# Kernel optimization log

Hardware: AMD Instinct MI355X
Metric: run time of the kernel (lower is better)

The kernel has to match this reference:

```python
import jax, jax.numpy as jnp
import numpy as np

NUM_HEADS = 4
INITIAL_VALUE = 1.0
HEADS_RANGE = 3.0


def rotate_every_two(x):
    x1 = x[..., ::2]
    x2 = x[..., 1::2]
    return jnp.stack([-x2, x1], axis=-1).reshape(x.shape)


def theta_shift(x, sin, cos):
    return x * cos + rotate_every_two(x) * sin


def rel_pos_2d(h, w, key_dim):
    # angle: repeat each frequency twice -> length key_dim
    base = 1.0 / 10000.0 ** jnp.linspace(0.0, 1.0, key_dim // 2)
    angle = jnp.repeat(base, 2)
    decay = jnp.log(1.0 - 2.0 ** (-(INITIAL_VALUE + HEADS_RANGE * jnp.arange(NUM_HEADS, dtype=jnp.float32) / NUM_HEADS)))
    idx = jnp.arange(h * w, dtype=jnp.float32)
    sin = jnp.sin(idx[:, None] * angle[None, :]).reshape(h, w, key_dim)
    cos = jnp.cos(idx[:, None] * angle[None, :]).reshape(h, w, key_dim)
    def decay_1d(l):
        i = jnp.arange(l, dtype=jnp.float32)
        return jnp.abs(i[:, None] - i[None, :])[None, :, :] * decay[:, None, None]  # (n, l, l)
    return sin, cos, decay_1d(h), decay_1d(w)


def setup_inputs() -> dict:
    key = jax.random.key(0)
    b, C, H, W = 16, 256, 64, 64
    ks = jax.random.split(key, 12)
    gain = 2.0 ** (-2.5)
    xav = (2.0 / (C + C)) ** 0.5
    return {
        "x": jax.random.normal(ks[0], (b, C, H, W), jnp.float32),
        "Wq": jax.random.normal(ks[1], (C, C), jnp.float32) * gain * xav,
        "bq": jnp.zeros((C,), jnp.float32),
        "Wk": jax.random.normal(ks[2], (C, C), jnp.float32) * gain * xav,
        "bk": jnp.zeros((C,), jnp.float32),
        "Wv": jax.random.normal(ks[3], (C, C), jnp.float32) * gain * xav,
        "bv": jnp.zeros((C,), jnp.float32),
        "dw_kernel": jax.random.normal(ks[4], (5, 5, 1, C), jnp.float32) * 0.05,
        "dw_bias": jnp.zeros((C,), jnp.float32),
        "Wo": jax.random.normal(ks[5], (C, C), jnp.float32) * xav,
        "bo": jnp.zeros((C,), jnp.float32),
    }


def reference(x, Wq, bq, Wk, bk, Wv, bv, dw_kernel, dw_bias, Wo, bo):
    x = jnp.transpose(x, (0, 2, 3, 1))  # (b, h, w, c)
    b, h, w, c = x.shape
    n = NUM_HEADS
    d = c // n  # key_dim == head_dim (value_factor=1)
    scaling = d ** (-0.5)

    sin, cos, mask_h, mask_w = rel_pos_2d(h, w, d)

    q = x @ Wq + bq
    k = (x @ Wk + bk) * scaling
    v = x @ Wv + bv  # (b, h, w, c)

    # depthwise 5x5 conv (lepe) on v, NHWC
    lepe = jax.lax.conv_general_dilated(
        v, dw_kernel, window_strides=(1, 1), padding=((2, 2), (2, 2)),
        dimension_numbers=("NHWC", "HWIO", "NHWC"), feature_group_count=c,
    ) + dw_bias

    q = q.reshape(b, h, w, n, d).transpose(0, 3, 1, 2, 4)  # (b, n, h, w, d)
    k = k.reshape(b, h, w, n, d).transpose(0, 3, 1, 2, 4)
    qr = theta_shift(q, sin, cos)  # sin/cos (h,w,d) broadcast
    kr = theta_shift(k, sin, cos)

    # width-axis attention: rows independent
    qr_w = qr.transpose(0, 2, 1, 3, 4)  # (b, h, n, w, d)
    kr_w = kr.transpose(0, 2, 1, 3, 4)
    v5 = v.reshape(b, h, w, n, d).transpose(0, 1, 3, 2, 4)  # (b, h, n, w, d)
    qk_w = jnp.einsum("bhnqd,bhnkd->bhnqk", qr_w, kr_w) + mask_w  # (b,h,n,w,w)
    v5 = jnp.einsum("bhnqk,bhnkd->bhnqd", jax.nn.softmax(qk_w, axis=-1), v5)

    # height-axis attention: columns independent
    qr_h = qr.transpose(0, 3, 1, 2, 4)  # (b, w, n, h, d)
    kr_h = kr.transpose(0, 3, 1, 2, 4)
    v6 = v5.transpose(0, 3, 2, 1, 4)  # (b, w, n, h, d)
    qk_h = jnp.einsum("bwnqd,bwnkd->bwnqk", qr_h, kr_h) + mask_h  # (b,w,n,h,h)
    out = jnp.einsum("bwnqk,bwnkd->bwnqd", jax.nn.softmax(qk_h, axis=-1), v6)

    out = out.transpose(0, 3, 1, 2, 4).reshape(b, h, w, c)  # (b,h,w,n*d)
    out = (out + lepe) @ Wo + bo
    return jnp.transpose(out, (0, 3, 1, 2))  # (b, c, h, w)
```

## Files before the change

### kernel.cpp

```cpp
#include <hip/hip_runtime.h>
#include <hip/hip_bf16.h>

typedef unsigned short u16;
typedef unsigned int   u32;
typedef __attribute__((ext_vector_type(8))) short bf16x8;
typedef __attribute__((ext_vector_type(4))) float f32x4;

__device__ __forceinline__ float bf2f(u16 u) {
    union { u32 i; float f; } x; x.i = ((u32)u) << 16; return x.f;
}
__device__ __forceinline__ u16 f2bf(float f) {
    union { float f; u32 i; } x; x.f = f;
    u32 i = x.i;
    u32 r = (i + 0x7fffu + ((i >> 16) & 1u)) >> 16;
    return (u16)r;
}

__global__ void k_tables(float* __restrict__ sinT, float* __restrict__ cosT) {
    int id = blockIdx.x * 256 + threadIdx.x;
    int t = id >> 5, i = id & 31;
    double ang = pow(10000.0, -(double)i / 31.0);
    double a = (double)t * ang;
    sinT[id] = (float)sin(a);
    cosT[id] = (float)cos(a);
}

__global__ __launch_bounds__(256) void k_prep_w(
    const float* __restrict__ Wq, const float* __restrict__ Wk,
    const float* __restrict__ Wv, const float* __restrict__ Wo,
    u16* __restrict__ WTq, u16* __restrict__ WTk,
    u16* __restrict__ WTv, u16* __restrict__ WoT)
{
    __shared__ float T[32][33];
    int z = blockIdx.z;
    const float* W = (z == 0) ? Wq : (z == 1) ? Wk : (z == 2) ? Wv : Wo;
    u16* WT        = (z == 0) ? WTq : (z == 1) ? WTk : (z == 2) ? WTv : WoT;
    int n0 = blockIdx.x * 32, k0 = blockIdx.y * 32;
    int tx = threadIdx.x & 31, ty = threadIdx.x >> 5;
#pragma unroll
    for (int i = 0; i < 4; i++)
        T[ty * 4 + i][tx] = W[(k0 + ty * 4 + i) * 256 + n0 + tx];
    __syncthreads();
#pragma unroll
    for (int i = 0; i < 4; i++)
        WT[(n0 + ty * 4 + i) * 256 + k0 + tx] = f2bf(T[tx][ty * 4 + i]);
}

__global__ __launch_bounds__(256) void k_prep_x(
    const float* __restrict__ x, u16* __restrict__ xT)
{
    __shared__ float T[32][33];
    int b = blockIdx.z, c0 = blockIdx.y * 32, s0 = blockIdx.x * 32;
    int tx = threadIdx.x & 31, ty = threadIdx.x >> 5;
#pragma unroll
    for (int i = 0; i < 4; i++)
        T[ty * 4 + i][tx] = x[((size_t)(b * 256 + c0 + ty * 4 + i)) * 4096 + s0 + tx];
    __syncthreads();
#pragma unroll
    for (int i = 0; i < 4; i++)
        xT[((size_t)(b * 4096 + s0 + ty * 4 + i)) * 256 + c0 + tx] = f2bf(T[tx][ty * 4 + i]);
}

__global__ __launch_bounds__(512, 1) void k_qkv_fused(
    const u16* __restrict__ xT, const u16* __restrict__ WTall,
    const float* __restrict__ bq, const float* __restrict__ bk,
    const float* __restrict__ bv,
    const float* __restrict__ sinT, const float* __restrict__ cosT,
    u16* __restrict__ qr, u16* __restrict__ kr, u16* __restrict__ vO)
{
    __shared__ alignas(16) u16 Alds[128 * 256];
    __shared__ alignas(16) u16 Blds[256 * 64];
    __shared__ float2 SL[128 * 32];

    const int tid = threadIdx.x;
    const int t0 = blockIdx.x * 128;

    const int ar = tid >> 5, ac = tid & 31;
    const int br = tid >> 3, bc = tid & 7;

    bf16x8 areg[8], breg[4];
#pragma unroll
    for (int p = 0; p < 8; ++p)
        areg[p] = *(const bf16x8*)(xT + (size_t)(t0 + p * 16 + ar) * 256 + ac * 8);
#pragma unroll
    for (int p = 0; p < 4; ++p)
        breg[p] = *(const bf16x8*)(WTall + (size_t)(p * 64 + br) * 256 + bc * 8);

#pragma unroll
    for (int p = 0; p < 8; ++p) {
        int r = p * 16 + ar;
        *(bf16x8*)(Alds + r * 256 + (ac ^ (r & 7)) * 8) = areg[p];
    }
    {
        const int sb = t0 & 4095;
#pragma unroll
        for (int p = 0; p < 8; ++p) {
            int idx = p * 512 + tid;
            int sl = idx >> 5, ii = idx & 31;
            SL[idx] = make_float2(cosT[(sb + sl) * 32 + ii], sinT[(sb + sl) * 32 + ii]);
        }
    }

    const int lane = tid & 63, w = tid >> 6;
    const int wr = w >> 2, wc = w & 3;
    const int l15 = lane & 15, l4 = lane >> 4, l7 = lane & 7;

#pragma unroll
    for (int mat = 0; mat < 3; ++mat) {
        f32x4 acc[4][4];
#pragma unroll
        for (int mi = 0; mi < 4; ++mi)
#pragma unroll
            for (int ni = 0; ni < 4; ++ni) acc[mi][ni] = (f32x4)0.f;

#pragma unroll
        for (int ks = 0; ks < 4; ++ks) {
            const int s = mat * 4 + ks;
            __syncthreads();
#pragma unroll
            for (int p = 0; p < 4; ++p) {
                int r = p * 64 + br;
                *(bf16x8*)(Blds + r * 64 + (bc ^ (r & 7)) * 8) = breg[p];
            }
            __syncthreads();
            if (s < 11) {
                const int s2 = s + 1;
                const int mat2 = s2 >> 2, ks2 = s2 & 3;
#pragma unroll
                for (int p = 0; p < 4; ++p)
                    breg[p] = *(const bf16x8*)(WTall + (size_t)mat2 * 65536 +
                                (size_t)(p * 64 + br) * 256 + ks2 * 64 + bc * 8);
            }
#pragma unroll
            for (int kk = 0; kk < 2; ++kk) {
                bf16x8 af[4], bfr[4];
#pragma unroll
                for (int mi = 0; mi < 4; ++mi) {
                    int r = wr * 64 + mi * 16 + l15;
                    af[mi] = *(const bf16x8*)(Alds + r * 256 + (ks * 8 + ((kk * 4 + l4) ^ l7)) * 8);
                }
#pragma unroll
                for (int ni = 0; ni < 4; ++ni) {
                    int r = wc * 64 + ni * 16 + l15;
                    bfr[ni] = *(const bf16x8*)(Blds + r * 64 + ((kk * 4 + l4) ^ l7) * 8);
                }
#pragma unroll
                for (int mi = 0; mi < 4; ++mi)
#pragma unroll
                    for (int ni = 0; ni < 4; ++ni)
                        acc[mi][ni] = __builtin_amdgcn_mfma_f32_16x16x32_bf16(
                            af[mi], bfr[ni], acc[mi][ni], 0, 0, 0);
            }
        }

        const float* bias = (mat == 0) ? bq : (mat == 1) ? bk : bv;
        u16* out          = (mat == 0) ? qr : (mat == 1) ? kr : vO;
        const float kscale = (mat == 1) ? 0.125f : 1.0f;
        float bcol[4]; int ip[4];
#pragma unroll
        for (int ni = 0; ni < 4; ++ni) {
            bcol[ni] = bias[wc * 64 + ni * 16 + l15];
            ip[ni] = (ni * 16 + l15) >> 1;
        }
#pragma unroll
        for (int mi = 0; mi < 4; ++mi) {
#pragma unroll
            for (int rg = 0; rg < 4; ++rg) {
                const int sl = wr * 64 + mi * 16 + l4 * 4 + rg;
                size_t trow = (size_t)(t0 + sl) * 256;
#pragma unroll
                for (int ni = 0; ni < 4; ++ni) {
                    float val = acc[mi][ni][rg] + bcol[ni];
                    float res;
                    if (mat != 2) {
                        val *= kscale;
                        float prt = __shfl_xor(val, 1);
                        float2 cs = SL[sl * 32 + ip[ni]];
                        res = (lane & 1) ? fmaf(val, cs.x,  prt * cs.y)
                                         : fmaf(val, cs.x, -prt * cs.y);
                    } else {
                        res = val;
                    }
                    float res2 = __shfl_xor(res, 1);
                    if (!(lane & 1)) {
                        u32 pk;
                        asm("v_cvt_pk_bf16_f32 %0, %1, %2" : "=v"(pk) : "v"(res), "v"(res2));
                        int o = wc * 64 + ni * 16 + l15;
                        *(u32*)(out + trow + o) = pk;
                    }
                }
            }
        }
    }
}

__global__ __launch_bounds__(256) void k_lepe(
    const u16* __restrict__ v, const float* __restrict__ dwk,
    const float* __restrict__ dwb, u16* __restrict__ lepe)
{
    __shared__ u16 VhU[12 * 12 * 64];
    __shared__ float Kl[25][64];
    const int b = blockIdx.z, cg = blockIdx.y * 64;
    const int ty0 = (blockIdx.x >> 3) * 8, tx0 = (blockIdx.x & 7) * 8;
    const int tid = threadIdx.x;

    for (int idx = tid; idx < 1600; idx += 256) {
        int tap = idx >> 6, c = idx & 63;
        Kl[tap][c] = dwk[tap * 256 + cg + c];
    }
#pragma unroll
    for (int p = 0; p < 9; ++p) {
        int idx = p * 256 + tid;
        int ch = idx & 15, pos = idx >> 4;
        int py = pos / 12, px = pos - py * 12;
        int gy = ty0 + py - 2, gx = tx0 + px - 2;
        ushort4 val = make_ushort4(0, 0, 0, 0);
        if (gy >= 0 && gy < 64 && gx >= 0 && gx < 64)
            val = *(const ushort4*)(v + (size_t)(b * 4096 + gy * 64 + gx) * 256 + cg + ch * 4);
        *(ushort4*)(VhU + pos * 64 + ch * 4) = val;
    }
    __syncthreads();

    const int c = tid & 63, pg = tid >> 6;
    float kreg[25];
#pragma unroll
    for (int t = 0; t < 25; t++) kreg[t] = Kl[t][c];
    const float bias = dwb[cg + c];

    float acc[2][8];
#pragma unroll
    for (int t = 0; t < 2; ++t)
#pragma unroll
        for (int ox = 0; ox < 8; ++ox) acc[t][ox] = bias;

#pragma unroll
    for (int rr = 0; rr < 6; ++rr) {
        const int r = pg * 2 + rr;
        float rv[12];
#pragma unroll
        for (int px = 0; px < 12; ++px)
            rv[px] = bf2f(VhU[(r * 12 + px) * 64 + c]);
        if (rr <= 4) {
            const int dy = rr;
#pragma unroll
            for (int ox = 0; ox < 8; ++ox)
#pragma unroll
                for (int dx = 0; dx < 5; ++dx)
                    acc[0][ox] = fmaf(rv[ox + dx], kreg[dy * 5 + dx], acc[0][ox]);
        }
        if (rr >= 1) {
            const int dy = rr - 1;
#pragma unroll
            for (int ox = 0; ox < 8; ++ox)
#pragma unroll
                for (int dx = 0; dx < 5; ++dx)
                    acc[1][ox] = fmaf(rv[ox + dx], kreg[dy * 5 + dx], acc[1][ox]);
        }
    }

#pragma unroll
    for (int t = 0; t < 2; ++t) {
        const int oy = pg * 2 + t;
#pragma unroll
        for (int ox = 0; ox < 8; ++ox)
            lepe[(size_t)(b * 4096 + (ty0 + oy) * 64 + tx0 + ox) * 256 + cg + c] =
                f2bf(acc[t][ox]);
    }
}

template <int AXIS>
__global__ __launch_bounds__(256) void k_attn_mfma(
    const u16* __restrict__ qr, const u16* __restrict__ kr,
    const u16* __restrict__ vsrc, const u16* __restrict__ lepeP,
    u16* __restrict__ outb)
{
    __shared__ u16 VT[4][64 * 72];
    __shared__ u16 PL[4][64 * 72];

    const int tid = threadIdx.x;
    const int w = tid >> 6, lane = tid & 63;
    const int l15 = lane & 15, l4 = lane >> 4;
    const int wid = blockIdx.x * 4 + w;
    const int b = wid >> 8, xy = (wid >> 2) & 63, n = wid & 3;

    size_t qkbase, vbase; int qkstride, vstride;
    if (AXIS == 0) {
        qkbase = ((size_t)(b * 4096 + xy * 64)) * 256 + n * 64;
        qkstride = 256;
        vbase = qkbase; vstride = 256;
    } else {
        qkbase = ((size_t)(b * 4096 + xy)) * 256 + n * 64;
        qkstride = 64 * 256;
        vbase = ((size_t)((b * 64 + xy) * 4 + n)) * 4096;
        vstride = 64;
    }

    u16* VTl = &VT[w][0];
    u16* PLl = &PL[w][0];

    bf16x8 vld[8];
    const int vrow = lane >> 3, vchunk = lane & 7;
#pragma unroll
    for (int it = 0; it < 8; ++it)
        vld[it] = *(const bf16x8*)(vsrc + vbase + (size_t)(it * 8 + vrow) * vstride + vchunk * 8);

    bf16x8 ka[4][2], qb[4][2];
#pragma unroll
    for (int t = 0; t < 4; ++t)
#pragma unroll
        for (int ks = 0; ks < 2; ++ks) {
            ka[t][ks] = *(const bf16x8*)(kr + qkbase + (size_t)(t * 16 + l15) * qkstride + ks * 32 + l4 * 8);
            qb[t][ks] = *(const bf16x8*)(qr + qkbase + (size_t)(t * 16 + l15) * qkstride + ks * 32 + l4 * 8);
        }

    f32x4 sacc[4][4];
#pragma unroll
    for (int kt = 0; kt < 4; ++kt)
#pragma unroll
        for (int qt = 0; qt < 4; ++qt) sacc[kt][qt] = (f32x4)0.f;
#pragma unroll
    for (int ks = 0; ks < 2; ++ks)
#pragma unroll
        for (int kt = 0; kt < 4; ++kt)
#pragma unroll
            for (int qt = 0; qt < 4; ++qt)
                sacc[kt][qt] = __builtin_amdgcn_mfma_f32_16x16x32_bf16(
                    ka[kt][ks], qb[qt][ks], sacc[kt][qt], 0, 0, 0);

#pragma unroll
    for (int it = 0; it < 8; ++it) {
        int gp = ((it ^ vchunk) << 3) + vrow;
#pragma unroll
        for (int j = 0; j < 8; ++j) {
            int d = vchunk * 8 + j;
            VTl[d * 72 + gp] = (u16)vld[it][j];
        }
    }

    const float decay = logf(1.0f - exp2f(-(1.0f + 0.75f * (float)n)));
#pragma unroll
    for (int qt = 0; qt < 4; ++qt) {
        const int qq = qt * 16 + l15;
        float lsum = 0.f;
#pragma unroll
        for (int kt = 0; kt < 4; ++kt) {
            const int kb = kt * 16 + l4 * 4;
#pragma unroll
            for (int rr = 0; rr < 4; ++rr) {
                float s = sacc[kt][qt][rr] + fabsf((float)(qq - kb - rr)) * decay;
                s = __expf(s);
                sacc[kt][qt][rr] = s;
                lsum += s;
            }
        }
        lsum += __shfl_xor(lsum, 16);
        lsum += __shfl_xor(lsum, 32);
        const float rinv = 1.0f / lsum;
#pragma unroll
        for (int kt = 0; kt < 4; ++kt) {
            float e0 = sacc[kt][qt][0] * rinv, e1 = sacc[kt][qt][1] * rinv;
            float e2 = sacc[kt][qt][2] * rinv, e3 = sacc[kt][qt][3] * rinv;
            u32 p0, p1;
            asm("v_cvt_pk_bf16_f32 %0, %1, %2" : "=v"(p0) : "v"(e0), "v"(e1));
            asm("v_cvt_pk_bf16_f32 %0, %1, %2" : "=v"(p1) : "v"(e2), "v"(e3));
            uint2 pp; pp.x = p0; pp.y = p1;
            *(uint2*)(PLl + (qt * 16 + l15) * 72 + kt * 16 + l4 * 4) = pp;
        }
    }

    __builtin_amdgcn_s_waitcnt(0xC07F);
    bf16x8 pa[4][2], vb[4][2];
#pragma unroll
    for (int qt = 0; qt < 4; ++qt)
#pragma unroll
        for (int ks = 0; ks < 2; ++ks)
            pa[qt][ks] = *(const bf16x8*)(PLl + (qt * 16 + l15) * 72 + ks * 32 + l4 * 8);
#pragma unroll
    for (int dt = 0; dt < 4; ++dt)
#pragma unroll
        for (int ks = 0; ks < 2; ++ks) {
            int d = dt * 16 + l15;
            int g = (ks * 4 + l4) ^ (d >> 3);
            vb[dt][ks] = *(const bf16x8*)(VTl + d * 72 + g * 8);
        }

    f32x4 oacc[4][4];
#pragma unroll
    for (int qt = 0; qt < 4; ++qt)
#pragma unroll
        for (int dt = 0; dt < 4; ++dt) oacc[qt][dt] = (f32x4)0.f;
#pragma unroll
    for (int ks = 0; ks < 2; ++ks)
#pragma unroll
        for (int qt = 0; qt < 4; ++qt)
#pragma unroll
            for (int dt = 0; dt < 4; ++dt)
                oacc[qt][dt] = __builtin_amdgcn_mfma_f32_16x16x32_bf16(
                    pa[qt][ks], vb[dt][ks], oacc[qt][dt], 0, 0, 0);

#pragma unroll
    for (int qt = 0; qt < 4; ++qt)
#pragma unroll
        for (int dt = 0; dt < 4; ++dt)
#pragma unroll
            for (int rr = 0; rr < 4; ++rr)
                PLl[(qt * 16 + l4 * 4 + rr) * 72 + dt * 16 + l15] = f2bf(oacc[qt][dt][rr]);
    __builtin_amdgcn_s_waitcnt(0xC07F);

    size_t orow;
    if (AXIS == 0) orow = ((size_t)((b * 64 + lane) * 4 + n)) * 4096 + xy * 64;
    else           orow = ((size_t)(b * 4096 + lane * 64 + xy)) * 256 + n * 64;
#pragma unroll
    for (int c = 0; c < 8; ++c) {
        bf16x8 o8 = *(const bf16x8*)(PLl + lane * 72 + c * 8);
        if (AXIS == 1) {
            bf16x8 lp = *(const bf16x8*)(lepeP + orow + c * 8);
            u16 hv[8];
#pragma unroll
            for (int j = 0; j < 8; ++j)
                hv[j] = f2bf(bf2f((u16)o8[j]) + bf2f((u16)lp[j]));
            o8 = *(bf16x8*)hv;
        }
        *(bf16x8*)(outb + orow + c * 8) = o8;
    }
}

__global__ __launch_bounds__(512, 1) void k_proj_fused(
    const u16* __restrict__ WoT, const u16* __restrict__ attnL,
    const float* __restrict__ bo, float* __restrict__ y)
{
    __shared__ alignas(16) u16 Alds[128 * 256];
    __shared__ alignas(16) u16 Blds[256 * 64];

    const int tid = threadIdx.x;
    const int bid = blockIdx.x;
    const int xcd = bid & 7, slot = bid >> 3;
    const int tt = xcd * 32 + (slot >> 1);
    const int oh = slot & 1;
    const int t0 = tt * 256;
    const int o0 = oh * 128;

    const int ar = tid >> 5, ac = tid & 31;
    const int br = tid >> 3, bc = tid & 7;

    bf16x8 areg[8], breg[4];
#pragma unroll
    for (int p = 0; p < 8; ++p)
        areg[p] = *(const bf16x8*)(WoT + (size_t)(o0 + p * 16 + ar) * 256 + ac * 8);
#pragma unroll
    for (int p = 0; p < 4; ++p)
        breg[p] = *(const bf16x8*)(attnL + (size_t)(t0 + p * 64 + br) * 256 + bc * 8);

#pragma unroll
    for (int p = 0; p < 8; ++p) {
        int r = p * 16 + ar;
        *(bf16x8*)(Alds + r * 256 + (ac ^ (r & 7)) * 8) = areg[p];
    }

    const int lane = tid & 63, w = tid >> 6;
    const int wr = w >> 2, wc = w & 3;
    const int l15 = lane & 15, l4 = lane >> 4, l7 = lane & 7;

    f32x4 acc[4][4];
#pragma unroll
    for (int mi = 0; mi < 4; ++mi)
#pragma unroll
        for (int ni = 0; ni < 4; ++ni) acc[mi][ni] = (f32x4)0.f;

#pragma unroll
    for (int ks = 0; ks < 4; ++ks) {
        __syncthreads();
#pragma unroll
        for (int p = 0; p < 4; ++p) {
            int r = p * 64 + br;
            *(bf16x8*)(Blds + r * 64 + (bc ^ (r & 7)) * 8) = breg[p];
        }
        __syncthreads();
        if (ks < 3) {
#pragma unroll
            for (int p = 0; p < 4; ++p)
                breg[p] = *(const bf16x8*)(attnL + (size_t)(t0 + p * 64 + br) * 256 + (ks + 1) * 64 + bc * 8);
        }
#pragma unroll
        for (int kk = 0; kk < 2; ++kk) {
            bf16x8 af[4], bfr[4];
#pragma unroll
            for (int mi = 0; mi < 4; ++mi) {
                int r = wr * 64 + mi * 16 + l15;
                af[mi] = *(const bf16x8*)(Alds + r * 256 + (ks * 8 + ((kk * 4 + l4) ^ l7)) * 8);
            }
#pragma unroll
            for (int ni = 0; ni < 4; ++ni) {
                int r = wc * 64 + ni * 16 + l15;
                bfr[ni] = *(const bf16x8*)(Blds + r * 64 + ((kk * 4 + l4) ^ l7) * 8);
            }
#pragma unroll
            for (int mi = 0; mi < 4; ++mi)
#pragma unroll
                for (int ni = 0; ni < 4; ++ni)
                    acc[mi][ni] = __builtin_amdgcn_mfma_f32_16x16x32_bf16(
                        af[mi], bfr[ni], acc[mi][ni], 0, 0, 0);
        }
    }

    const int b = t0 >> 12, sb = t0 & 4095;
#pragma unroll
    for (int mi = 0; mi < 4; ++mi) {
#pragma unroll
        for (int rg = 0; rg < 4; ++rg) {
            int o = o0 + wr * 64 + mi * 16 + l4 * 4 + rg;
            float bb = bo[o];
            float* yrow = y + ((size_t)(b * 256 + o)) * 4096 + sb + wc * 64;
#pragma unroll
            for (int ni = 0; ni < 4; ++ni)
                yrow[ni * 16 + l15] = acc[mi][ni][rg] + bb;
        }
    }
}

extern "C" void kernel_launch(void* const* d_in, const int* in_sizes, int n_in,
                              void* d_out, int out_size, void* d_ws, size_t ws_size,
                              hipStream_t stream)
{
    const float* x   = (const float*)d_in[0];
    const float* Wq  = (const float*)d_in[1];
    const float* bq  = (const float*)d_in[2];
    const float* Wk  = (const float*)d_in[3];
    const float* bk  = (const float*)d_in[4];
    const float* Wv  = (const float*)d_in[5];
    const float* bv  = (const float*)d_in[6];
    const float* dwk = (const float*)d_in[7];
    const float* dwb = (const float*)d_in[8];
    const float* Wo  = (const float*)d_in[9];
    const float* bo  = (const float*)d_in[10];
    float* y = (float*)d_out;

    char* ws = (char*)d_ws;
    const size_t MB = 1024 * 1024;
    float* sinT = (float*)(ws);
    float* cosT = (float*)(ws + 512 * 1024);
    u16* WTq = (u16*)(ws + 1 * MB);
    u16* WTk = WTq + 65536;
    u16* WTv = WTk + 65536;
    u16* WoT = WTv + 65536;
    u16* qr   = (u16*)(ws + 2 * MB);
    u16* kr   = (u16*)(ws + 2 * MB + 32 * MB);
    u16* v    = (u16*)(ws + 2 * MB + 64 * MB);
    u16* lepe = (u16*)(ws + 2 * MB + 96 * MB);
    u16* xT   = (u16*)(ws + 2 * MB + 128 * MB);
    u16* v5   = xT;
    u16* attn = v;

    k_tables<<<dim3(512), dim3(256), 0, stream>>>(sinT, cosT);
    k_prep_w<<<dim3(8, 8, 4), dim3(256), 0, stream>>>(Wq, Wk, Wv, Wo, WTq, WTk, WTv, WoT);
    k_prep_x<<<dim3(128, 8, 16), dim3(256), 0, stream>>>(x, xT);
    k_qkv_fused<<<dim3(512), dim3(512), 0, stream>>>(
        xT, WTq, bq, bk, bv, sinT, cosT, qr, kr, v);
    k_lepe<<<dim3(64, 4, 16), dim3(256), 0, stream>>>(v, dwk, dwb, lepe);
    k_attn_mfma<0><<<dim3(1024), dim3(256), 0, stream>>>(qr, kr, v, nullptr, v5);
    k_attn_mfma<1><<<dim3(1024), dim3(256), 0, stream>>>(qr, kr, v5, lepe, attn);
    k_proj_fused<<<dim3(512), dim3(512), 0, stream>>>(WoT, attn, bo, y);
}
```

Measured before the change: 213.0 us.

## Load GEMM B operands directly from global memory, drop B and sin/cos LDS staging

In both the QKV and output-projection GEMMs, the B operand is now read straight from global memory into MFMA fragments instead of being staged through a swizzled LDS tile with two barriers per k-step. The sin/cos tables are interleaved into one float2 table that the rotary epilogue reads directly from global memory. Launch bounds rise from 1 to 4 blocks per unit. The aim is to remove the per-step barriers and shrink LDS use so more blocks fit. In exchange there is no register prefetch of B, fragment loads are uncoalesced 16-byte strided reads that rely on cache, and a larger occupancy target may limit registers.

```diff
diff --git a/kernel.cpp b/kernel.cpp
--- a/kernel.cpp
+++ b/kernel.cpp
@@ -16,13 +16,12 @@
     return (u16)r;
 }
 
-__global__ void k_tables(float* __restrict__ sinT, float* __restrict__ cosT) {
+__global__ void k_tables(float2* __restrict__ csT) {
     int id = blockIdx.x * 256 + threadIdx.x;
     int t = id >> 5, i = id & 31;
     double ang = pow(10000.0, -(double)i / 31.0);
     double a = (double)t * ang;
-    sinT[id] = (float)sin(a);
-    cosT[id] = (float)cos(a);
+    csT[id] = make_float2((float)cos(a), (float)sin(a));
 }
 
 __global__ __launch_bounds__(256) void k_prep_w(
@@ -61,52 +60,40 @@
         xT[((size_t)(b * 4096 + s0 + ty * 4 + i)) * 256 + c0 + tx] = f2bf(T[tx][ty * 4 + i]);
 }
 
-__global__ __launch_bounds__(512, 1) void k_qkv_fused(
+__global__ __launch_bounds__(512, 4) void k_qkv_fused(
     const u16* __restrict__ xT, const u16* __restrict__ WTall,
     const float* __restrict__ bq, const float* __restrict__ bk,
     const float* __restrict__ bv,
-    const float* __restrict__ sinT, const float* __restrict__ cosT,
+    const float2* __restrict__ csT,
     u16* __restrict__ qr, u16* __restrict__ kr, u16* __restrict__ vO)
 {
     __shared__ alignas(16) u16 Alds[128 * 256];
-    __shared__ alignas(16) u16 Blds[256 * 64];
-    __shared__ float2 SL[128 * 32];
 
     const int tid = threadIdx.x;
     const int t0 = blockIdx.x * 128;
-
     const int ar = tid >> 5, ac = tid & 31;
-    const int br = tid >> 3, bc = tid & 7;
-
-    bf16x8 areg[8], breg[4];
-#pragma unroll
-    for (int p = 0; p < 8; ++p)
-        areg[p] = *(const bf16x8*)(xT + (size_t)(t0 + p * 16 + ar) * 256 + ac * 8);
-#pragma unroll
-    for (int p = 0; p < 4; ++p)
-        breg[p] = *(const bf16x8*)(WTall + (size_t)(p * 64 + br) * 256 + bc * 8);
-
-#pragma unroll
-    for (int p = 0; p < 8; ++p) {
-        int r = p * 16 + ar;
-        *(bf16x8*)(Alds + r * 256 + (ac ^ (r & 7)) * 8) = areg[p];
-    }
+
     {
-        const int sb = t0 & 4095;
+        bf16x8 areg[8];
+#pragma unroll
+        for (int p = 0; p < 8; ++p)
+            areg[p] = *(const bf16x8*)(xT + (size_t)(t0 + p * 16 + ar) * 256 + ac * 8);
 #pragma unroll
         for (int p = 0; p < 8; ++p) {
-            int idx = p * 512 + tid;
-            int sl = idx >> 5, ii = idx & 31;
-            SL[idx] = make_float2(cosT[(sb + sl) * 32 + ii], sinT[(sb + sl) * 32 + ii]);
-        }
-    }
+            int r = p * 16 + ar;
+            *(bf16x8*)(Alds + r * 256 + (ac ^ (r & 7)) * 8) = areg[p];
+        }
+    }
+    __syncthreads();
 
     const int lane = tid & 63, w = tid >> 6;
     const int wr = w >> 2, wc = w & 3;
     const int l15 = lane & 15, l4 = lane >> 4, l7 = lane & 7;
+    const int sb = t0 & 4095;
 
 #pragma unroll
     for (int mat = 0; mat < 3; ++mat) {
+        const u16* Wm = WTall + (size_t)mat * 65536;
         f32x4 acc[4][4];
 #pragma unroll
         for (int mi = 0; mi < 4; ++mi)
@@ -115,34 +102,17 @@
 
 #pragma unroll
         for (int ks = 0; ks < 4; ++ks) {
-            const int s = mat * 4 + ks;
-            __syncthreads();
-#pragma unroll
-            for (int p = 0; p < 4; ++p) {
-                int r = p * 64 + br;
-                *(bf16x8*)(Blds + r * 64 + (bc ^ (r & 7)) * 8) = breg[p];
-            }
-            __syncthreads();
-            if (s < 11) {
-                const int s2 = s + 1;
-                const int mat2 = s2 >> 2, ks2 = s2 & 3;
-#pragma unroll
-                for (int p = 0; p < 4; ++p)
-                    breg[p] = *(const bf16x8*)(WTall + (size_t)mat2 * 65536 +
-                                (size_t)(p * 64 + br) * 256 + ks2 * 64 + bc * 8);
-            }
 #pragma unroll
             for (int kk = 0; kk < 2; ++kk) {
                 bf16x8 af[4], bfr[4];
+#pragma unroll
+                for (int ni = 0; ni < 4; ++ni)
+                    bfr[ni] = *(const bf16x8*)(Wm +
+                        (size_t)(wc * 64 + ni * 16 + l15) * 256 + ks * 64 + kk * 32 + l4 * 8);
 #pragma unroll
                 for (int mi = 0; mi < 4; ++mi) {
                     int r = wr * 64 + mi * 16 + l15;
                     af[mi] = *(const bf16x8*)(Alds + r * 256 + (ks * 8 + ((kk * 4 + l4) ^ l7)) * 8);
-                }
-#pragma unroll
-                for (int ni = 0; ni < 4; ++ni) {
-                    int r = wc * 64 + ni * 16 + l15;
-                    bfr[ni] = *(const bf16x8*)(Blds + r * 64 + ((kk * 4 + l4) ^ l7) * 8);
                 }
 #pragma unroll
                 for (int mi = 0; mi < 4; ++mi)
@@ -175,7 +145,7 @@
                     if (mat != 2) {
                         val *= kscale;
                         float prt = __shfl_xor(val, 1);
-                        float2 cs = SL[sl * 32 + ip[ni]];
+                        float2 cs = csT[(size_t)(sb + sl) * 32 + ip[ni]];
                         res = (lane & 1) ? fmaf(val, cs.x,  prt * cs.y)
                                          : fmaf(val, cs.x, -prt * cs.y);
                     } else {
@@ -425,12 +395,11 @@
     }
 }
 
-__global__ __launch_bounds__(512, 1) void k_proj_fused(
+__global__ __launch_bounds__(512, 4) void k_proj_fused(
     const u16* __restrict__ WoT, const u16* __restrict__ attnL,
     const float* __restrict__ bo, float* __restrict__ y)
 {
     __shared__ alignas(16) u16 Alds[128 * 256];
-    __shared__ alignas(16) u16 Blds[256 * 64];
 
     const int tid = threadIdx.x;
     const int bid = blockIdx.x;
@@ -441,21 +410,19 @@
     const int o0 = oh * 128;
 
     const int ar = tid >> 5, ac = tid & 31;
-    const int br = tid >> 3, bc = tid & 7;
-
-    bf16x8 areg[8], breg[4];
-#pragma unroll
-    for (int p = 0; p < 8; ++p)
-        areg[p] = *(const bf16x8*)(WoT + (size_t)(o0 + p * 16 + ar) * 256 + ac * 8);
-#pragma unroll
-    for (int p = 0; p < 4; ++p)
-        breg[p] = *(const bf16x8*)(attnL + (size_t)(t0 + p * 64 + br) * 256 + bc * 8);
-
-#pragma unroll
-    for (int p = 0; p < 8; ++p) {
-        int r = p * 16 + ar;
-        *(bf16x8*)(Alds + r * 256 + (ac ^ (r & 7)) * 8) = areg[p];
-    }
+
+    {
+        bf16x8 areg[8];
+#pragma unroll
+        for (int p = 0; p < 8; ++p)
+            areg[p] = *(const bf16x8*)(WoT + (size_t)(o0 + p * 16 + ar) * 256 + ac * 8);
+#pragma unroll
+        for (int p = 0; p < 8; ++p) {
+            int r = p * 16 + ar;
+            *(bf16x8*)(Alds + r * 256 + (ac ^ (r & 7)) * 8) = areg[p];
+        }
+    }
+    __syncthreads();
 
     const int lane = tid & 63, w = tid >> 6;
     const int wr = w >> 2, wc = w & 3;
@@ -469,30 +436,17 @@
 
 #pragma unroll
     for (int ks = 0; ks < 4; ++ks) {
-        __syncthreads();
-#pragma unroll
-        for (int p = 0; p < 4; ++p) {
-            int r = p * 64 + br;
-            *(bf16x8*)(Blds + r * 64 + (bc ^ (r & 7)) * 8) = breg[p];
-        }
-        __syncthreads();
-        if (ks < 3) {
-#pragma unroll
-            for (int p = 0; p < 4; ++p)
-                breg[p] = *(const bf16x8*)(attnL + (size_t)(t0 + p * 64 + br) * 256 + (ks + 1) * 64 + bc * 8);
-        }
 #pragma unroll
         for (int kk = 0; kk < 2; ++kk) {
             bf16x8 af[4], bfr[4];
+#pragma unroll
+            for (int ni = 0; ni < 4; ++ni)
+                bfr[ni] = *(const bf16x8*)(attnL +
+                    (size_t)(t0 + wc * 64 + ni * 16 + l15) * 256 + ks * 64 + kk * 32 + l4 * 8);
 #pragma unroll
             for (int mi = 0; mi < 4; ++mi) {
                 int r = wr * 64 + mi * 16 + l15;
                 af[mi] = *(const bf16x8*)(Alds + r * 256 + (ks * 8 + ((kk * 4 + l4) ^ l7)) * 8);
-            }
-#pragma unroll
-            for (int ni = 0; ni < 4; ++ni) {
-                int r = wc * 64 + ni * 16 + l15;
-                bfr[ni] = *(const bf16x8*)(Blds + r * 64 + ((kk * 4 + l4) ^ l7) * 8);
             }
 #pragma unroll
             for (int mi = 0; mi < 4; ++mi)
@@ -537,8 +491,7 @@
 
     char* ws = (char*)d_ws;
     const size_t MB = 1024 * 1024;
-    float* sinT = (float*)(ws);
-    float* cosT = (float*)(ws + 512 * 1024);
+    float2* csT = (float2*)(ws);
     u16* WTq = (u16*)(ws + 1 * MB);
     u16* WTk = WTq + 65536;
     u16* WTv = WTk + 65536;
@@ -551,11 +504,11 @@
     u16* v5   = xT;
     u16* attn = v;
 
-    k_tables<<<dim3(512), dim3(256), 0, stream>>>(sinT, cosT);
+    k_tables<<<dim3(512), dim3(256), 0, stream>>>(csT);
     k_prep_w<<<dim3(8, 8, 4), dim3(256), 0, stream>>>(Wq, Wk, Wv, Wo, WTq, WTk, WTv, WoT);
     k_prep_x<<<dim3(128, 8, 16), dim3(256), 0, stream>>>(x, xT);
     k_qkv_fused<<<dim3(512), dim3(512), 0, stream>>>(
-        xT, WTq, bq, bk, bv, sinT, cosT, qr, kr, v);
+        xT, WTq, bq, bk, bv, csT, qr, kr, v);
     k_lepe<<<dim3(64, 4, 16), dim3(256), 0, stream>>>(v, dwk, dwb, lepe);
     k_attn_mfma<0><<<dim3(1024), dim3(256), 0, stream>>>(qr, kr, v, nullptr, v5);
     k_attn_mfma<1><<<dim3(1024), dim3(256), 0, stream>>>(qr, kr, v5, lepe, attn);
```

After: 284.4 us. 1.34x slower.
